# Kernel optimization log

Hardware: AMD Instinct MI355X
Metric: run time of the kernel (lower is better)

## Reference

```python
import jax, jax.numpy as jnp
import numpy as np

H = 1024
V = 50257
S = 20


def setup_inputs() -> dict:
    key = jax.random.key(0)
    ks = jax.random.split(key, 13)
    sc = 0.02
    return {
        "token": jax.random.randint(ks[0], (1,), 0, V),
        "hidden": jax.random.normal(ks[1], (1, 1, H), jnp.float32),
        "encoder_outputs": jax.random.normal(ks[2], (S, 1, H), jnp.float32),
        "embed_table": jax.random.normal(ks[3], (V, H), jnp.float32) * sc,
        "attn_w": jax.random.normal(ks[4], (H, 2 * H), jnp.float32) * sc,
        "attn_b": jax.random.normal(ks[5], (H,), jnp.float32) * sc,
        "v_w": jax.random.normal(ks[6], (1, H), jnp.float32) * sc,
        "gru_w_ih": jax.random.normal(ks[7], (3 * H, 2 * H), jnp.float32) * sc,
        "gru_w_hh": jax.random.normal(ks[8], (3 * H, H), jnp.float32) * sc,
        "gru_b_ih": jax.random.normal(ks[9], (3 * H,), jnp.float32) * sc,
        "gru_b_hh": jax.random.normal(ks[10], (3 * H,), jnp.float32) * sc,
        "out_w": jax.random.normal(ks[11], (V, H), jnp.float32) * sc,
        "out_b": jax.random.normal(ks[12], (V,), jnp.float32) * sc,
    }


def reference(token, hidden, encoder_outputs, embed_table, attn_w, attn_b, v_w,
              gru_w_ih, gru_w_hh, gru_b_ih, gru_b_hh, out_w, out_b):
    s = encoder_outputs.shape[0]
    # embedding lookup -> [1,1,H]
    embed = embed_table[token].reshape(1, 1, -1)
    enc = jnp.transpose(encoder_outputs, (1, 0, 2))  # [1,S,H]
    h_rep = jnp.broadcast_to(hidden, (1, s, hidden.shape[-1]))  # repeat over src_len
    # Bahdanau additive attention
    energy = jnp.tanh(jnp.concatenate([h_rep, enc], axis=2) @ attn_w.T + attn_b)  # [1,S,H]
    scores = jnp.squeeze(energy @ v_w.T, axis=2)  # [1,S]
    attn = jax.nn.softmax(scores, axis=1)[:, None, :]  # [1,1,S]
    weighted = jnp.einsum('bqs,bsh->bqh', attn, enc)  # [1,1,H]
    # single-step GRU (PyTorch gate layout: r,z,n)
    x = jnp.concatenate([embed, weighted], axis=2)[0]  # [1,2H]
    h0 = hidden[0]  # [1,H]
    gi = x @ gru_w_ih.T + gru_b_ih  # [1,3H]
    gh = h0 @ gru_w_hh.T + gru_b_hh  # [1,3H]
    i_r, i_z, i_n = jnp.split(gi, 3, axis=1)
    h_r, h_z, h_n = jnp.split(gh, 3, axis=1)
    r = jax.nn.sigmoid(i_r + h_r)
    z = jax.nn.sigmoid(i_z + h_z)
    n = jnp.tanh(i_n + r * h_n)
    h_new = (1.0 - z) * n + z * h0  # [1,H]
    prediction = jax.nn.log_softmax(h_new @ out_w.T + out_b, axis=1)  # [1,V]
    return prediction, h_new[None]  # ([1,V], [1,1,H])
```

## Files before the change

### kernel.cpp

```cpp
#include <hip/hip_runtime.h>
#include <math.h>

#define H 1024
#define S 20
#define V 50257

__device__ __forceinline__ float wave_reduce_sum(float v) {
  #pragma unroll
  for (int off = 32; off > 0; off >>= 1)
    v += __shfl_xor(v, off, 64);
  return v;
}

__global__ __launch_bounds__(256) void kA(
    const int* __restrict__ token,
    const float* __restrict__ hidden,
    const float* __restrict__ enc,
    const float* __restrict__ embed_table,
    const float* __restrict__ attn_w,
    const float* __restrict__ attn_b,
    const float* __restrict__ v_w,
    const float* __restrict__ w_ih,
    const float* __restrict__ w_hh,
    const float* __restrict__ b_ih,
    const float* __restrict__ b_hh,
    float* __restrict__ bpart,
    float* __restrict__ gie,
    float* __restrict__ ghv)
{
  __shared__ float esh[4][S];
  const int t = threadIdx.x;
  const int lane = t & 63;
  const int wv = t >> 6;
  const int b = blockIdx.x;

  if (b < 256) {
    const int j = b * 4 + wv;
    const float* wrow = attn_w + (size_t)j * (2 * H);
    float4 wlo[4], whi[4], hid4[4];
    #pragma unroll
    for (int q = 0; q < 4; ++q) {
      const int idx = lane + 64 * q;
      wlo[q]  = ((const float4*)wrow)[idx];
      whi[q]  = ((const float4*)(wrow + H))[idx];
      hid4[q] = ((const float4*)hidden)[idx];
    }
    float hp = 0.f;
    #pragma unroll
    for (int q = 0; q < 4; ++q)
      hp += wlo[q].x * hid4[q].x + wlo[q].y * hid4[q].y +
            wlo[q].z * hid4[q].z + wlo[q].w * hid4[q].w;
    hp = wave_reduce_sum(hp);

    float myval = 0.f;
    #pragma unroll
    for (int s = 0; s < S; ++s) {
      const float4* e4 = (const float4*)(enc + s * H);
      float es = 0.f;
      #pragma unroll
      for (int q = 0; q < 4; ++q) {
        const int idx = lane + 64 * q;
        const float4 e = e4[idx];
        es += whi[q].x * e.x + whi[q].y * e.y + whi[q].z * e.z + whi[q].w * e.w;
      }
      es = wave_reduce_sum(es);
      if (lane == s) myval = es;
    }
    if (lane < S)
      esh[wv][lane] = tanhf(hp + myval + attn_b[j]) * v_w[j];
    __syncthreads();
    if (wv == 0 && lane < S)
      bpart[lane * 256 + b] =
          esh[0][lane] + esh[1][lane] + esh[2][lane] + esh[3][lane];
  } else if (b < 1024) {
    const int W = (b - 256) * 4 + wv;
    const float* wr = w_ih + (size_t)W * (2 * H);
    const float* embed = embed_table + (size_t)(*token) * H;
    float a = 0.f;
    #pragma unroll
    for (int q = 0; q < 4; ++q) {
      const int idx = lane + 64 * q;
      const float4 w = ((const float4*)wr)[idx];
      const float4 e = ((const float4*)embed)[idx];
      a += w.x * e.x + w.y * e.y + w.z * e.z + w.w * e.w;
    }
    a = wave_reduce_sum(a);
    if (lane == 0) gie[W] = a + b_ih[W];
  } else {
    const int W = (b - 1024) * 4 + wv;
    const float* wr = w_hh + (size_t)W * H;
    float a = 0.f;
    #pragma unroll
    for (int q = 0; q < 4; ++q) {
      const int idx = lane + 64 * q;
      const float4 w = ((const float4*)wr)[idx];
      const float4 h = ((const float4*)hidden)[idx];
      a += w.x * h.x + w.y * h.y + w.z * h.z + w.w * h.w;
    }
    a = wave_reduce_sum(a);
    if (lane == 0) ghv[W] = a + b_hh[W];
  }
}

__global__ __launch_bounds__(256) void kB(
    const float* __restrict__ enc,
    const float* __restrict__ bpart,
    const float* __restrict__ w_ih,
    const float* __restrict__ gie,
    float* __restrict__ gi_full)
{
  __shared__ float scores_sh[S];
  __shared__ float attn_sh[S];
  __shared__ float wsh[H];
  const int t = threadIdx.x;
  const int lane = t & 63;
  const int wv = t >> 6;

  for (int s = wv; s < S; s += 4) {
    const float4 p = ((const float4*)(bpart + s * 256))[lane];
    float v = p.x + p.y + p.z + p.w;
    v = wave_reduce_sum(v);
    if (lane == 0) scores_sh[s] = v;
  }
  __syncthreads();
  if (t == 0) {
    float m = -1e30f;
    for (int s = 0; s < S; ++s) m = fmaxf(m, scores_sh[s]);
    float sum = 0.f;
    for (int s = 0; s < S; ++s) {
      const float e = expf(scores_sh[s] - m);
      attn_sh[s] = e;
      sum += e;
    }
    const float inv = 1.f / sum;
    for (int s = 0; s < S; ++s) attn_sh[s] *= inv;
  }
  __syncthreads();
  for (int h = t; h < H; h += 256) {
    float acc = 0.f;
    #pragma unroll
    for (int s = 0; s < S; ++s) acc += attn_sh[s] * enc[s * H + h];
    wsh[h] = acc;
  }
  __syncthreads();

  const int W = blockIdx.x * 4 + wv;
  const float* wr = w_ih + (size_t)W * (2 * H) + H;
  float a = 0.f;
  #pragma unroll
  for (int q = 0; q < 4; ++q) {
    const int idx = lane + 64 * q;
    const float4 w = ((const float4*)wr)[idx];
    const float4 x = ((const float4*)wsh)[idx];
    a += w.x * x.x + w.y * x.y + w.z * x.z + w.w * x.w;
  }
  a = wave_reduce_sum(a);
  if (lane == 0) gi_full[W] = gie[W] + a;
}

__global__ __launch_bounds__(512) void kC(
    const float* __restrict__ hidden,
    const float* __restrict__ gi_full,
    const float* __restrict__ ghv,
    const float* __restrict__ out_w,
    const float* __restrict__ out_b,
    float* __restrict__ out,
    float* __restrict__ pmax,
    float* __restrict__ psum)
{
  __shared__ float hnew_lds[H];
  __shared__ float stat_m[8];
  __shared__ float stat_s[8];
  const int t = threadIdx.x;
  const int lane = t & 63;
  const int wv = t >> 6;
  const int b = blockIdx.x;

  #pragma unroll
  for (int r = 0; r < 2; ++r) {
    const int j = t + r * 512;
    const float i_r = gi_full[j];
    const float i_z = gi_full[H + j];
    const float i_n = gi_full[2 * H + j];
    const float h_r = ghv[j];
    const float h_z = ghv[H + j];
    const float h_n = ghv[2 * H + j];
    const float rr = 1.f / (1.f + expf(-(i_r + h_r)));
    const float zz = 1.f / (1.f + expf(-(i_z + h_z)));
    const float nn = tanhf(i_n + rr * h_n);
    const float hn = (1.f - zz) * nn + zz * hidden[j];
    hnew_lds[j] = hn;
    if (b == 0) out[V + j] = hn;
  }
  __syncthreads();

  float4 h4[4];
  #pragma unroll
  for (int q = 0; q < 4; ++q)
    h4[q] = ((const float4*)hnew_lds)[lane + 64 * q];

  const int W = b * 8 + wv;
  const int vbase = W * 4;
  const int v0 = (vbase < V - 1) ? vbase : (V - 1);
  const int v1 = (vbase + 1 < V) ? vbase + 1 : (V - 1);
  const int v2 = (vbase + 2 < V) ? vbase + 2 : (V - 1);
  const int v3 = (vbase + 3 < V) ? vbase + 3 : (V - 1);
  const float4* r0 = (const float4*)(out_w + (size_t)v0 * H);
  const float4* r1 = (const float4*)(out_w + (size_t)v1 * H);
  const float4* r2 = (const float4*)(out_w + (size_t)v2 * H);
  const float4* r3 = (const float4*)(out_w + (size_t)v3 * H);
  float a0 = 0.f, a1 = 0.f, a2 = 0.f, a3 = 0.f;
  #pragma unroll
  for (int q = 0; q < 4; ++q) {
    const int idx = lane + 64 * q;
    const float4 w0 = r0[idx];
    const float4 w1 = r1[idx];
    const float4 w2 = r2[idx];
    const float4 w3 = r3[idx];
    a0 += w0.x * h4[q].x + w0.y * h4[q].y + w0.z * h4[q].z + w0.w * h4[q].w;
    a1 += w1.x * h4[q].x + w1.y * h4[q].y + w1.z * h4[q].z + w1.w * h4[q].w;
    a2 += w2.x * h4[q].x + w2.y * h4[q].y + w2.z * h4[q].z + w2.w * h4[q].w;
    a3 += w3.x * h4[q].x + w3.y * h4[q].y + w3.z * h4[q].z + w3.w * h4[q].w;
  }
  a0 = wave_reduce_sum(a0);
  a1 = wave_reduce_sum(a1);
  a2 = wave_reduce_sum(a2);
  a3 = wave_reduce_sum(a3);
  float val0 = (vbase     < V) ? a0 + out_b[v0] : -INFINITY;
  float val1 = (vbase + 1 < V) ? a1 + out_b[v1] : -INFINITY;
  float val2 = (vbase + 2 < V) ? a2 + out_b[v2] : -INFINITY;
  float val3 = (vbase + 3 < V) ? a3 + out_b[v3] : -INFINITY;

  if (lane == 0) {
    if (vbase + 3 < V) {
      float4 o; o.x = val0; o.y = val1; o.z = val2; o.w = val3;
      *reinterpret_cast<float4*>(out + vbase) = o;
    } else {
      if (vbase     < V) out[vbase]     = val0;
      if (vbase + 1 < V) out[vbase + 1] = val1;
      if (vbase + 2 < V) out[vbase + 2] = val2;
      if (vbase + 3 < V) out[vbase + 3] = val3;
    }
  }

  float m = fmaxf(fmaxf(val0, val1), fmaxf(val2, val3));
  float s = 0.f;
  if (m != -INFINITY) {
    s = expf(val0 - m) + expf(val1 - m) + expf(val2 - m) + expf(val3 - m);
  }
  if (lane == 0) { stat_m[wv] = m; stat_s[wv] = s; }
  __syncthreads();
  if (t == 0) {
    float M = stat_m[0], Ss = stat_s[0];
    #pragma unroll
    for (int i = 1; i < 8; ++i) {
      const float m2 = stat_m[i], s2 = stat_s[i];
      const float M2 = fmaxf(M, m2);
      Ss = Ss * expf(M - M2) + s2 * expf(m2 - M2);
      M = M2;
    }
    pmax[b] = M;
    psum[b] = Ss;
  }
}

__global__ __launch_bounds__(1024) void kD(
    const float* __restrict__ pmax,
    const float* __restrict__ psum, int n,
    float* __restrict__ out)
{
  __shared__ float sm[16];
  __shared__ float ss[16];
  __shared__ float Tsh;
  const int t = threadIdx.x, lane = t & 63, wv = t >> 6;

  float dm = -INFINITY, dsv = 0.f;
  for (int i = t; i < n; i += 1024) {
    const float pm = pmax[i];
    const float ps = psum[i];
    const float M2 = fmaxf(dm, pm);
    dsv = dsv * expf(dm - M2) + ps * expf(pm - M2);
    dm = M2;
  }
  #pragma unroll
  for (int off = 32; off > 0; off >>= 1) {
    const float m2 = __shfl_xor(dm, off, 64);
    const float s2 = __shfl_xor(dsv, off, 64);
    const float M2 = fmaxf(dm, m2);
    dsv = dsv * expf(dm - M2) + s2 * expf(m2 - M2);
    dm = M2;
  }
  if (lane == 0) { sm[wv] = dm; ss[wv] = dsv; }
  __syncthreads();
  if (t == 0) {
    float M = sm[0], Ss = ss[0];
    #pragma unroll
    for (int i = 1; i < 16; ++i) {
      const float m2 = sm[i], s2 = ss[i];
      const float M2 = fmaxf(M, m2);
      Ss = Ss * expf(M - M2) + s2 * expf(m2 - M2);
      M = M2;
    }
    Tsh = M + logf(Ss);
  }
  __syncthreads();
  const float T = Tsh;
  const int i = blockIdx.x * 1024 + t;
  if (i < V) out[i] -= T;
}

extern "C" void kernel_launch(void* const* d_in, const int* in_sizes, int n_in,
                              void* d_out, int out_size, void* d_ws, size_t ws_size,
                              hipStream_t stream) {
  const int*   token       = (const int*)d_in[0];
  const float* hidden      = (const float*)d_in[1];
  const float* enc         = (const float*)d_in[2];
  const float* embed_table = (const float*)d_in[3];
  const float* attn_w      = (const float*)d_in[4];
  const float* attn_b      = (const float*)d_in[5];
  const float* v_w         = (const float*)d_in[6];
  const float* w_ih        = (const float*)d_in[7];
  const float* w_hh        = (const float*)d_in[8];
  const float* b_ih        = (const float*)d_in[9];
  const float* b_hh        = (const float*)d_in[10];
  const float* out_w       = (const float*)d_in[11];
  const float* out_b       = (const float*)d_in[12];
  float* out = (float*)d_out;
  float* ws  = (float*)d_ws;

  float* bpart   = ws;
  float* gie     = ws + 5120;
  float* ghv     = ws + 8192;
  float* gi_full = ws + 11264;
  float* pmax    = ws + 14336;
  float* psum    = ws + 15936;

  const int nblkC = (V + 31) / 32;

  kA<<<1792, 256, 0, stream>>>(token, hidden, enc, embed_table, attn_w, attn_b,
                               v_w, w_ih, w_hh, b_ih, b_hh, bpart, gie, ghv);
  kB<<<768, 256, 0, stream>>>(enc, bpart, w_ih, gie, gi_full);
  kC<<<nblkC, 512, 0, stream>>>(hidden, gi_full, ghv, out_w, out_b, out, pmax, psum);
  kD<<<(V + 1023) / 1024, 1024, 0, stream>>>(pmax, psum, nblkC, out);
}
```

Before: 64.50 us.

## Fuse GRU gates into kB and make kC persistent with grid-stride rows

kB now computes all three gate dot products for each hidden unit and applies the GRU update itself, writing h_new once. This removes the per-block recomputation of the gates that every kC block used to do. kC launches a fixed 512 blocks that grid-stride over vocab row groups and keep an online max/sum per wave. That shrinks the partial-stat array so kD can reduce it in a single pass of 512 threads. The cost is that kB runs fewer blocks doing three times the work each, and kC has fewer resident waves available to hide memory latency while streaming out_w.

```diff
diff --git a/kernel.cpp b/kernel.cpp
--- a/kernel.cpp
+++ b/kernel.cpp
@@ -4,6 +4,9 @@
 #define H 1024
 #define S 20
 #define V 50257
+#define NGRP ((V + 3) / 4)
+#define KC_BLOCKS 512
+#define KC_WAVES (KC_BLOCKS * 8)
 
 __device__ __forceinline__ float wave_reduce_sum(float v) {
   #pragma unroll
@@ -107,7 +110,10 @@
     const float* __restrict__ bpart,
     const float* __restrict__ w_ih,
     const float* __restrict__ gie,
-    float* __restrict__ gi_full)
+    const float* __restrict__ ghv,
+    const float* __restrict__ hidden,
+    float* __restrict__ hnew,
+    float* __restrict__ out)
 {
   __shared__ float scores_sh[S];
   __shared__ float attn_sh[S];
@@ -115,6 +121,7 @@
   const int t = threadIdx.x;
   const int lane = t & 63;
   const int wv = t >> 6;
+  const int j = blockIdx.x * 4 + wv;
 
   for (int s = wv; s < S; s += 4) {
     const float4 p = ((const float4*)(bpart + s * 256))[lane];
@@ -144,111 +151,113 @@
   }
   __syncthreads();
 
-  const int W = blockIdx.x * 4 + wv;
-  const float* wr = w_ih + (size_t)W * (2 * H) + H;
-  float a = 0.f;
-  #pragma unroll
-  for (int q = 0; q < 4; ++q) {
-    const int idx = lane + 64 * q;
-    const float4 w = ((const float4*)wr)[idx];
-    const float4 x = ((const float4*)wsh)[idx];
-    a += w.x * x.x + w.y * x.y + w.z * x.z + w.w * x.w;
-  }
-  a = wave_reduce_sum(a);
-  if (lane == 0) gi_full[W] = gie[W] + a;
+  float4 c4[4];
+  #pragma unroll
+  for (int q = 0; q < 4; ++q) c4[q] = ((const float4*)wsh)[lane + 64 * q];
+
+  float gict[3];
+  #pragma unroll
+  for (int g = 0; g < 3; ++g) {
+    const float* wr = w_ih + (size_t)(g * H + j) * (2 * H) + H;
+    float a = 0.f;
+    #pragma unroll
+    for (int q = 0; q < 4; ++q) {
+      const float4 w = ((const float4*)wr)[lane + 64 * q];
+      a += w.x * c4[q].x + w.y * c4[q].y + w.z * c4[q].z + w.w * c4[q].w;
+    }
+    gict[g] = wave_reduce_sum(a);
+  }
+
+  if (lane == 0) {
+    const float i_r = gie[j]         + gict[0];
+    const float i_z = gie[H + j]     + gict[1];
+    const float i_n = gie[2 * H + j] + gict[2];
+    const float h_r = ghv[j];
+    const float h_z = ghv[H + j];
+    const float h_n = ghv[2 * H + j];
+    const float r = 1.f / (1.f + expf(-(i_r + h_r)));
+    const float z = 1.f / (1.f + expf(-(i_z + h_z)));
+    const float n = tanhf(i_n + r * h_n);
+    const float hn = (1.f - z) * n + z * hidden[j];
+    hnew[j] = hn;
+    out[V + j] = hn;
+  }
 }
 
 __global__ __launch_bounds__(512) void kC(
-    const float* __restrict__ hidden,
-    const float* __restrict__ gi_full,
-    const float* __restrict__ ghv,
+    const float* __restrict__ hnew,
     const float* __restrict__ out_w,
     const float* __restrict__ out_b,
     float* __restrict__ out,
     float* __restrict__ pmax,
     float* __restrict__ psum)
 {
-  __shared__ float hnew_lds[H];
   __shared__ float stat_m[8];
   __shared__ float stat_s[8];
   const int t = threadIdx.x;
   const int lane = t & 63;
   const int wv = t >> 6;
   const int b = blockIdx.x;
-
-  #pragma unroll
-  for (int r = 0; r < 2; ++r) {
-    const int j = t + r * 512;
-    const float i_r = gi_full[j];
-    const float i_z = gi_full[H + j];
-    const float i_n = gi_full[2 * H + j];
-    const float h_r = ghv[j];
-    const float h_z = ghv[H + j];
-    const float h_n = ghv[2 * H + j];
-    const float rr = 1.f / (1.f + expf(-(i_r + h_r)));
-    const float zz = 1.f / (1.f + expf(-(i_z + h_z)));
-    const float nn = tanhf(i_n + rr * h_n);
-    const float hn = (1.f - zz) * nn + zz * hidden[j];
-    hnew_lds[j] = hn;
-    if (b == 0) out[V + j] = hn;
-  }
-  __syncthreads();
+  const int gw = b * 8 + wv;
 
   float4 h4[4];
   #pragma unroll
   for (int q = 0; q < 4; ++q)
-    h4[q] = ((const float4*)hnew_lds)[lane + 64 * q];
-
-  const int W = b * 8 + wv;
-  const int vbase = W * 4;
-  const int v0 = (vbase < V - 1) ? vbase : (V - 1);
-  const int v1 = (vbase + 1 < V) ? vbase + 1 : (V - 1);
-  const int v2 = (vbase + 2 < V) ? vbase + 2 : (V - 1);
-  const int v3 = (vbase + 3 < V) ? vbase + 3 : (V - 1);
-  const float4* r0 = (const float4*)(out_w + (size_t)v0 * H);
-  const float4* r1 = (const float4*)(out_w + (size_t)v1 * H);
-  const float4* r2 = (const float4*)(out_w + (size_t)v2 * H);
-  const float4* r3 = (const float4*)(out_w + (size_t)v3 * H);
-  float a0 = 0.f, a1 = 0.f, a2 = 0.f, a3 = 0.f;
-  #pragma unroll
-  for (int q = 0; q < 4; ++q) {
-    const int idx = lane + 64 * q;
-    const float4 w0 = r0[idx];
-    const float4 w1 = r1[idx];
-    const float4 w2 = r2[idx];
-    const float4 w3 = r3[idx];
-    a0 += w0.x * h4[q].x + w0.y * h4[q].y + w0.z * h4[q].z + w0.w * h4[q].w;
-    a1 += w1.x * h4[q].x + w1.y * h4[q].y + w1.z * h4[q].z + w1.w * h4[q].w;
-    a2 += w2.x * h4[q].x + w2.y * h4[q].y + w2.z * h4[q].z + w2.w * h4[q].w;
-    a3 += w3.x * h4[q].x + w3.y * h4[q].y + w3.z * h4[q].z + w3.w * h4[q].w;
-  }
-  a0 = wave_reduce_sum(a0);
-  a1 = wave_reduce_sum(a1);
-  a2 = wave_reduce_sum(a2);
-  a3 = wave_reduce_sum(a3);
-  float val0 = (vbase     < V) ? a0 + out_b[v0] : -INFINITY;
-  float val1 = (vbase + 1 < V) ? a1 + out_b[v1] : -INFINITY;
-  float val2 = (vbase + 2 < V) ? a2 + out_b[v2] : -INFINITY;
-  float val3 = (vbase + 3 < V) ? a3 + out_b[v3] : -INFINITY;
-
-  if (lane == 0) {
-    if (vbase + 3 < V) {
-      float4 o; o.x = val0; o.y = val1; o.z = val2; o.w = val3;
-      *reinterpret_cast<float4*>(out + vbase) = o;
-    } else {
-      if (vbase     < V) out[vbase]     = val0;
-      if (vbase + 1 < V) out[vbase + 1] = val1;
-      if (vbase + 2 < V) out[vbase + 2] = val2;
-      if (vbase + 3 < V) out[vbase + 3] = val3;
-    }
-  }
-
-  float m = fmaxf(fmaxf(val0, val1), fmaxf(val2, val3));
-  float s = 0.f;
-  if (m != -INFINITY) {
-    s = expf(val0 - m) + expf(val1 - m) + expf(val2 - m) + expf(val3 - m);
-  }
-  if (lane == 0) { stat_m[wv] = m; stat_s[wv] = s; }
+    h4[q] = ((const float4*)hnew)[lane + 64 * q];
+
+  float wm = -INFINITY, wsum = 0.f;
+
+  for (int grp = gw; grp < NGRP; grp += KC_WAVES) {
+    const int vbase = grp * 4;
+    const int v0 = vbase;
+    const int v1 = (vbase + 1 < V) ? vbase + 1 : (V - 1);
+    const int v2 = (vbase + 2 < V) ? vbase + 2 : (V - 1);
+    const int v3 = (vbase + 3 < V) ? vbase + 3 : (V - 1);
+    const float4* r0 = (const float4*)(out_w + (size_t)v0 * H);
+    const float4* r1 = (const float4*)(out_w + (size_t)v1 * H);
+    const float4* r2 = (const float4*)(out_w + (size_t)v2 * H);
+    const float4* r3 = (const float4*)(out_w + (size_t)v3 * H);
+    float a0 = 0.f, a1 = 0.f, a2 = 0.f, a3 = 0.f;
+    #pragma unroll
+    for (int q = 0; q < 4; ++q) {
+      const int idx = lane + 64 * q;
+      const float4 w0 = r0[idx];
+      const float4 w1 = r1[idx];
+      const float4 w2 = r2[idx];
+      const float4 w3 = r3[idx];
+      a0 += w0.x * h4[q].x + w0.y * h4[q].y + w0.z * h4[q].z + w0.w * h4[q].w;
+      a1 += w1.x * h4[q].x + w1.y * h4[q].y + w1.z * h4[q].z + w1.w * h4[q].w;
+      a2 += w2.x * h4[q].x + w2.y * h4[q].y + w2.z * h4[q].z + w2.w * h4[q].w;
+      a3 += w3.x * h4[q].x + w3.y * h4[q].y + w3.z * h4[q].z + w3.w * h4[q].w;
+    }
+    a0 = wave_reduce_sum(a0);
+    a1 = wave_reduce_sum(a1);
+    a2 = wave_reduce_sum(a2);
+    a3 = wave_reduce_sum(a3);
+    const float val0 = a0 + out_b[v0];
+    const float val1 = (vbase + 1 < V) ? a1 + out_b[v1] : -INFINITY;
+    const float val2 = (vbase + 2 < V) ? a2 + out_b[v2] : -INFINITY;
+    const float val3 = (vbase + 3 < V) ? a3 + out_b[v3] : -INFINITY;
+
+    if (lane == 0) {
+      if (vbase + 3 < V) {
+        float4 o; o.x = val0; o.y = val1; o.z = val2; o.w = val3;
+        *reinterpret_cast<float4*>(out + vbase) = o;
+      } else {
+        out[vbase] = val0;
+        if (vbase + 1 < V) out[vbase + 1] = val1;
+        if (vbase + 2 < V) out[vbase + 2] = val2;
+      }
+    }
+
+    const float gm = fmaxf(fmaxf(val0, val1), fmaxf(val2, val3));
+    const float M2 = fmaxf(wm, gm);
+    wsum = wsum * expf(wm - M2) +
+           expf(val0 - M2) + expf(val1 - M2) + expf(val2 - M2) + expf(val3 - M2);
+    wm = M2;
+  }
+
+  if (lane == 0) { stat_m[wv] = wm; stat_s[wv] = wsum; }
   __syncthreads();
   if (t == 0) {
     float M = stat_m[0], Ss = stat_s[0];
@@ -264,24 +273,18 @@
   }
 }
 
-__global__ __launch_bounds__(1024) void kD(
+__global__ __launch_bounds__(512) void kD(
     const float* __restrict__ pmax,
-    const float* __restrict__ psum, int n,
+    const float* __restrict__ psum,
     float* __restrict__ out)
 {
-  __shared__ float sm[16];
-  __shared__ float ss[16];
+  __shared__ float sm[8];
+  __shared__ float ss[8];
   __shared__ float Tsh;
   const int t = threadIdx.x, lane = t & 63, wv = t >> 6;
 
-  float dm = -INFINITY, dsv = 0.f;
-  for (int i = t; i < n; i += 1024) {
-    const float pm = pmax[i];
-    const float ps = psum[i];
-    const float M2 = fmaxf(dm, pm);
-    dsv = dsv * expf(dm - M2) + ps * expf(pm - M2);
-    dm = M2;
-  }
+  float dm = pmax[t];
+  float dsv = psum[t];
   #pragma unroll
   for (int off = 32; off > 0; off >>= 1) {
     const float m2 = __shfl_xor(dm, off, 64);
@@ -295,7 +298,7 @@
   if (t == 0) {
     float M = sm[0], Ss = ss[0];
     #pragma unroll
-    for (int i = 1; i < 16; ++i) {
+    for (int i = 1; i < 8; ++i) {
       const float m2 = sm[i], s2 = ss[i];
       const float M2 = fmaxf(M, m2);
       Ss = Ss * expf(M - M2) + s2 * expf(m2 - M2);
@@ -305,7 +308,7 @@
   }
   __syncthreads();
   const float T = Tsh;
-  const int i = blockIdx.x * 1024 + t;
+  const int i = blockIdx.x * 512 + t;
   if (i < V) out[i] -= T;
 }
 
@@ -328,18 +331,16 @@
   float* out = (float*)d_out;
   float* ws  = (float*)d_ws;
 
-  float* bpart   = ws;
-  float* gie     = ws + 5120;
-  float* ghv     = ws + 8192;
-  float* gi_full = ws + 11264;
-  float* pmax    = ws + 14336;
-  float* psum    = ws + 15936;
-
-  const int nblkC = (V + 31) / 32;
+  float* bpart = ws;
+  float* gie   = ws + 5120;
+  float* ghv   = ws + 8192;
+  float* hnew  = ws + 11264;
+  float* pmax  = ws + 12288;
+  float* psum  = ws + 12800;
 
   kA<<<1792, 256, 0, stream>>>(token, hidden, enc, embed_table, attn_w, attn_b,
                                v_w, w_ih, w_hh, b_ih, b_hh, bpart, gie, ghv);
-  kB<<<768, 256, 0, stream>>>(enc, bpart, w_ih, gie, gi_full);
-  kC<<<nblkC, 512, 0, stream>>>(hidden, gi_full, ghv, out_w, out_b, out, pmax, psum);
-  kD<<<(V + 1023) / 1024, 1024, 0, stream>>>(pmax, psum, nblkC, out);
-}
+  kB<<<256, 256, 0, stream>>>(enc, bpart, w_ih, gie, ghv, hidden, hnew, out);
+  kC<<<KC_BLOCKS, 512, 0, stream>>>(hnew, out_w, out_b, out, pmax, psum);
+  kD<<<(V + 511) / 512, 512, 0, stream>>>(pmax, psum, out);
+}
```

After: 60.84 us. 5.7% less time.
